# Kernel tuning notes

Hardware: AMD Instinct MI355X
Metric: run time of the kernel (lower is better)

## Reference

```python
import jax, jax.numpy as jnp
import numpy as np

EPS = 1e-06

def setup_inputs() -> dict:
    key = jax.random.key(0)
    k1, k2, k3, k4 = jax.random.split(key, 4)
    B, N, H, W = 8, 8, 512, 512
    pd_rgbo = jax.random.normal(k1, (B, 4, H, W), dtype=jnp.float32)
    gt_rgbo = jax.random.normal(k2, (B, 4, H, W), dtype=jnp.float32)
    pd_mask = jax.random.randint(k3, (B, N, H, W), 0, 2, dtype=jnp.int32)
    gt_mask = jax.random.randint(k4, (B, N, H, W), 0, 2, dtype=jnp.int32)
    return {"pd_rgbo": pd_rgbo, "gt_rgbo": gt_rgbo, "pd_mask": pd_mask, "gt_mask": gt_mask}

def reference(pd_rgbo, gt_rgbo, pd_mask, gt_mask):
    # masks -> bool, derived mask combinations
    pm = pd_mask.astype(bool)            # [B,N,H,W]
    gm = gt_mask.astype(bool)
    dt = pd_rgbo.dtype
    pmf = pm.astype(dt)
    and_f = (pm & gm).astype(dt)         # logical_and
    xor_f = (pm & ~gm).astype(dt)        # xor(or, gt) == pd & ~gt
    gmf = gm.astype(dt)

    pd_rgb = pd_rgbo[:, :3]              # [B,3,H,W]
    gt_rgb = gt_rgbo[:, :3]
    pd_o = jnp.round(pd_rgbo[:, 3])      # [B,H,W]
    gt_o = jnp.round(gt_rgbo[:, 3])

    # per-pixel L2 color distance over channels: [B,H,W]
    diff_norm = jnp.linalg.norm(pd_rgb - gt_rgb, ord=2, axis=1)

    # punish: mean color distance over predicted-mask pixels (per b,n)
    sim_sum = jnp.einsum('bhw,bnhw->bn', diff_norm, pmf)
    count = jnp.sum(pmf, axis=(2, 3))
    punish = sim_sum / (count + EPS)

    # IoU from rounded opacities masked by logical masks
    inter = jnp.einsum('bhw,bnhw->bn', pd_o, and_f)
    gt_sum = jnp.einsum('bhw,bnhw->bn', gt_o, gmf)
    pd_xor_sum = jnp.einsum('bhw,bnhw->bn', pd_o, xor_f)
    iou = inter / (gt_sum + pd_xor_sum + EPS)

    # weights default to ones -> plain mean over all (b, n) pairs
    loss = jnp.mean(1.0 - iou + punish)
    return loss
```

## Files before the change

### kernel.cpp

```cpp
#include <hip/hip_runtime.h>


constexpr int Bc  = 8;
constexpr int Nc  = 8;
constexpr int HWc = 512 * 512;
constexpr int BPI = 512;
constexpr float EPSc = 1e-6f;

__device__ __forceinline__ float2 gload_f2(const float* a) {
    float2 r;
    asm volatile("global_load_dwordx2 %0, %1, off" : "=v"(r) : "v"(a) : "memory");
    return r;
}
__device__ __forceinline__ int4 gload_i4(const int* a) {
    int4 r;
    asm volatile("global_load_dwordx4 %0, %1, off" : "=v"(r) : "v"(a) : "memory");
    return r;
}
#define WAITV(n_) do {                                                   \
        asm volatile("s_waitcnt vmcnt(" #n_ ")" ::: "memory");           \
        __builtin_amdgcn_sched_barrier(0);                               \
    } while (0)

__device__ __forceinline__ float wave_reduce(float v) {
#pragma unroll
    for (int off = 32; off; off >>= 1) v += __shfl_xor(v, off, 64);
    return v;
}

template<bool USE_PART>
__global__ __launch_bounds__(256, 4) void niou_partial(
    const float* __restrict__ pd, const float* __restrict__ gt,
    const int* __restrict__ pmask, const int* __restrict__ gmask,
    float* __restrict__ outp )
{
    __shared__ float dnL[512], poL[512], goL[512];

    const int tid  = threadIdx.x;
    const int b    = blockIdx.x >> 9;
    const int blk  = blockIdx.x & 511;
    const int base = blk * 512;

    const float* pdB = pd + (size_t)b * 4 * HWc + base + 2 * tid;
    const float* gtB = gt + (size_t)b * 4 * HWc + base + 2 * tid;
    float2 pr[4], gr[4];
#pragma unroll
    for (int c = 0; c < 4; ++c) pr[c] = gload_f2(pdB + (size_t)c * HWc);
#pragma unroll
    for (int c = 0; c < 4; ++c) gr[c] = gload_f2(gtB + (size_t)c * HWc);

    const int g = tid >> 6, q = tid & 63;
    int4 pmv[2][2], gmv[2][2];
#pragma unroll
    for (int pp = 0; pp < 2; ++pp) {
        const size_t pl = (size_t)(b * Nc + 2 * g + pp) * HWc + base + 4 * q;
#pragma unroll
        for (int qq = 0; qq < 2; ++qq) {
            pmv[pp][qq] = gload_i4(pmask + pl + 256 * qq);
            gmv[pp][qq] = gload_i4(gmask + pl + 256 * qq);
        }
    }

    WAITV(8);
    {
        const float dx0 = pr[0].x - gr[0].x, dy0 = pr[1].x - gr[1].x, dz0 = pr[2].x - gr[2].x;
        const float dx1 = pr[0].y - gr[0].y, dy1 = pr[1].y - gr[1].y, dz1 = pr[2].y - gr[2].y;
        float2 d2, p2, g2;
        d2.x = sqrtf(dx0*dx0 + dy0*dy0 + dz0*dz0);
        d2.y = sqrtf(dx1*dx1 + dy1*dy1 + dz1*dz1);
        p2.x = rintf(pr[3].x); p2.y = rintf(pr[3].y);
        g2.x = rintf(gr[3].x); g2.y = rintf(gr[3].y);
        *reinterpret_cast<float2*>(&dnL[2 * tid]) = d2;
        *reinterpret_cast<float2*>(&poL[2 * tid]) = p2;
        *reinterpret_cast<float2*>(&goL[2 * tid]) = g2;
    }
    __syncthreads();

    WAITV(0);
    float4 dnq[2], poq[2], goq[2];
#pragma unroll
    for (int qq = 0; qq < 2; ++qq) {
        const int li = 256 * qq + 4 * q;
        dnq[qq] = *reinterpret_cast<const float4*>(&dnL[li]);
        poq[qq] = *reinterpret_cast<const float4*>(&poL[li]);
        goq[qq] = *reinterpret_cast<const float4*>(&goL[li]);
    }

    float acc[2][4];
    int   wcnt[2];
#pragma unroll
    for (int pp = 0; pp < 2; ++pp) {
        wcnt[pp] = 0;
#pragma unroll
        for (int k = 0; k < 4; ++k) acc[pp][k] = 0.f;
    }

#pragma unroll
    for (int pp = 0; pp < 2; ++pp)
#pragma unroll
        for (int qq = 0; qq < 2; ++qq) {
            const int pmx[4] = {pmv[pp][qq].x, pmv[pp][qq].y, pmv[pp][qq].z, pmv[pp][qq].w};
            const int gmx[4] = {gmv[pp][qq].x, gmv[pp][qq].y, gmv[pp][qq].z, gmv[pp][qq].w};
            const float dnj[4] = {dnq[qq].x, dnq[qq].y, dnq[qq].z, dnq[qq].w};
            const float poj[4] = {poq[qq].x, poq[qq].y, poq[qq].z, poq[qq].w};
            const float goj[4] = {goq[qq].x, goq[qq].y, goq[qq].z, goq[qq].w};
#pragma unroll
            for (int j = 0; j < 4; ++j) {
                const bool P = pmx[j] != 0;
                const bool G = gmx[j] != 0;
                wcnt[pp] += __popcll(__ballot(P));
                const float s = P ? poj[j] : 0.f;
                acc[pp][0] += P ? dnj[j] : 0.f;
                acc[pp][1] += G ? s      : 0.f;
                acc[pp][2] += G ? goj[j] : 0.f;
                acc[pp][3] += s;
            }
        }

    const int lane = tid & 63;
#pragma unroll
    for (int pp = 0; pp < 2; ++pp) {
        const float s0 = wave_reduce(acc[pp][0]);
        const float s1 = wave_reduce(acc[pp][1]);
        const float s2 = wave_reduce(acc[pp][2]);
        const float s3 = wave_reduce(acc[pp][3]);
        if (lane == 0) {
            const int n = 2 * g + pp;
            if (USE_PART) {
                float* dst = outp + (size_t)(b * 40 + n * 5) * BPI + blk;
                dst[0 * BPI] = s0;
                dst[1 * BPI] = (float)wcnt[pp];
                dst[2 * BPI] = s1;
                dst[3 * BPI] = s2;
                dst[4 * BPI] = s3;
            } else {
                float* wsn = outp + (size_t)(b * 40 + n * 5) * 16;
                atomicAdd(&wsn[0 * 16], s0);
                atomicAdd(&wsn[1 * 16], (float)wcnt[pp]);
                atomicAdd(&wsn[2 * 16], s1);
                atomicAdd(&wsn[3 * 16], s2);
                atomicAdd(&wsn[4 * 16], s3);
            }
        }
    }
}

__global__ __launch_bounds__(256) void niou_reduce(
    const float* __restrict__ part, float* __restrict__ sums)
{
    const int slot = blockIdx.x;
    const int tid  = threadIdx.x;
    float s = 0.f;
#pragma unroll
    for (int i = 0; i < BPI; i += 256) s += part[(size_t)slot * BPI + i + tid];
    s = wave_reduce(s);
    __shared__ float w4[4];
    if ((tid & 63) == 0) w4[tid >> 6] = s;
    __syncthreads();
    if (tid == 0) sums[slot] = w4[0] + w4[1] + w4[2] + w4[3];
}

__global__ __launch_bounds__(64) void niou_final(
    const float* __restrict__ w0, float* __restrict__ out, int pad)
{
    const int t = threadIdx.x;
    const float* w = w0 + (size_t)t * 5 * pad;
    const float sim   = w[0 * pad];
    const float cnt   = w[1 * pad];
    const float inter = w[2 * pad];
    const float gts   = w[3 * pad];
    const float ssum  = w[4 * pad];
    const float xo    = ssum - inter;
    const float punish = sim / (cnt + EPSc);
    const float iou    = inter / (gts + xo + EPSc);
    float term = 1.0f - iou + punish;
#pragma unroll
    for (int off = 32; off; off >>= 1) term += __shfl_xor(term, off, 64);
    if (t == 0) out[0] = term * (1.0f / 64.0f);
}

extern "C" void kernel_launch(void* const* d_in, const int* in_sizes, int n_in,
                              void* d_out, int out_size, void* d_ws, size_t ws_size,
                              hipStream_t stream) {
    const float* pd_rgbo = (const float*)d_in[0];
    const float* gt_rgbo = (const float*)d_in[1];
    const int*   pd_mask = (const int*)d_in[2];
    const int*   gt_mask = (const int*)d_in[3];
    float* out = (float*)d_out;
    float* ws  = (float*)d_ws;

    const size_t need = ((size_t)320 * BPI + 320) * sizeof(float);
    if (ws_size >= need) {
        float* part = ws;
        float* sums = ws + (size_t)320 * BPI;
        niou_partial<true><<<Bc * BPI, 256, 0, stream>>>(pd_rgbo, gt_rgbo,
                                                         pd_mask, gt_mask, part);
        niou_reduce<<<320, 256, 0, stream>>>(part, sums);
        niou_final<<<1, 64, 0, stream>>>(sums, out, 1);
    } else {
        hipMemsetAsync(ws, 0, 320 * 16 * sizeof(float), stream);
        niou_partial<false><<<Bc * BPI, 256, 0, stream>>>(pd_rgbo, gt_rgbo,
                                                          pd_mask, gt_mask, ws);
        niou_final<<<1, 64, 0, stream>>>(ws, out, 16);
    }
}
```

Baseline: 38.61 us.

## Replace partial-sum buffer and reduce kernel with atomics; split mask wait

Drops the two-pass reduction (per-block partial writes plus a separate reduce kernel) and always accumulates per-(b,n) sums with float atomics into a zeroed, padded workspace, preceded by a memset. This removes one kernel launch and the partial-buffer traffic, at the cost of contention from 512 blocks atomically adding to each of 320 slots. It also splits the final vmcnt wait so the first mask plane pair is processed while the second is still in flight. Float atomics make the summation order nondeterministic.

Result: slower. 59.00 us (+52.8%).

```diff
diff --git a/kernel.cpp b/kernel.cpp
--- a/kernel.cpp
+++ b/kernel.cpp
@@ -5,6 +5,7 @@
 constexpr int Nc  = 8;
 constexpr int HWc = 512 * 512;
 constexpr int BPI = 512;
+constexpr int PAD = 16;
 constexpr float EPSc = 1e-6f;
 
 __device__ __forceinline__ float2 gload_f2(const float* a) {
@@ -28,11 +29,10 @@
     return v;
 }
 
-template<bool USE_PART>
 __global__ __launch_bounds__(256, 4) void niou_partial(
     const float* __restrict__ pd, const float* __restrict__ gt,
     const int* __restrict__ pmask, const int* __restrict__ gmask,
-    float* __restrict__ outp )
+    float* __restrict__ ws )
 {
     __shared__ float dnL[512], poL[512], goL[512];
 
@@ -76,7 +76,6 @@
     }
     __syncthreads();
 
-    WAITV(0);
     float4 dnq[2], poq[2], goq[2];
 #pragma unroll
     for (int qq = 0; qq < 2; ++qq) {
@@ -96,7 +95,8 @@
     }
 
 #pragma unroll
-    for (int pp = 0; pp < 2; ++pp)
+    for (int pp = 0; pp < 2; ++pp) {
+        if (pp == 0) WAITV(4); else WAITV(0);
 #pragma unroll
         for (int qq = 0; qq < 2; ++qq) {
             const int pmx[4] = {pmv[pp][qq].x, pmv[pp][qq].y, pmv[pp][qq].z, pmv[pp][qq].w};
@@ -116,6 +116,7 @@
                 acc[pp][3] += s;
             }
         }
+    }
 
     const int lane = tid & 63;
 #pragma unroll
@@ -126,50 +127,26 @@
         const float s3 = wave_reduce(acc[pp][3]);
         if (lane == 0) {
             const int n = 2 * g + pp;
-            if (USE_PART) {
-                float* dst = outp + (size_t)(b * 40 + n * 5) * BPI + blk;
-                dst[0 * BPI] = s0;
-                dst[1 * BPI] = (float)wcnt[pp];
-                dst[2 * BPI] = s1;
-                dst[3 * BPI] = s2;
-                dst[4 * BPI] = s3;
-            } else {
-                float* wsn = outp + (size_t)(b * 40 + n * 5) * 16;
-                atomicAdd(&wsn[0 * 16], s0);
-                atomicAdd(&wsn[1 * 16], (float)wcnt[pp]);
-                atomicAdd(&wsn[2 * 16], s1);
-                atomicAdd(&wsn[3 * 16], s2);
-                atomicAdd(&wsn[4 * 16], s3);
-            }
+            float* wsn = ws + (size_t)(b * 40 + n * 5) * PAD;
+            atomicAdd(&wsn[0 * PAD], s0);
+            atomicAdd(&wsn[1 * PAD], (float)wcnt[pp]);
+            atomicAdd(&wsn[2 * PAD], s1);
+            atomicAdd(&wsn[3 * PAD], s2);
+            atomicAdd(&wsn[4 * PAD], s3);
         }
     }
 }
 
-__global__ __launch_bounds__(256) void niou_reduce(
-    const float* __restrict__ part, float* __restrict__ sums)
-{
-    const int slot = blockIdx.x;
-    const int tid  = threadIdx.x;
-    float s = 0.f;
-#pragma unroll
-    for (int i = 0; i < BPI; i += 256) s += part[(size_t)slot * BPI + i + tid];
-    s = wave_reduce(s);
-    __shared__ float w4[4];
-    if ((tid & 63) == 0) w4[tid >> 6] = s;
-    __syncthreads();
-    if (tid == 0) sums[slot] = w4[0] + w4[1] + w4[2] + w4[3];
-}
-
 __global__ __launch_bounds__(64) void niou_final(
-    const float* __restrict__ w0, float* __restrict__ out, int pad)
+    const float* __restrict__ w0, float* __restrict__ out)
 {
     const int t = threadIdx.x;
-    const float* w = w0 + (size_t)t * 5 * pad;
-    const float sim   = w[0 * pad];
-    const float cnt   = w[1 * pad];
-    const float inter = w[2 * pad];
-    const float gts   = w[3 * pad];
-    const float ssum  = w[4 * pad];
+    const float* w = w0 + (size_t)t * 5 * PAD;
+    const float sim   = w[0 * PAD];
+    const float cnt   = w[1 * PAD];
+    const float inter = w[2 * PAD];
+    const float gts   = w[3 * PAD];
+    const float ssum  = w[4 * PAD];
     const float xo    = ssum - inter;
     const float punish = sim / (cnt + EPSc);
     const float iou    = inter / (gts + xo + EPSc);
@@ -189,18 +166,7 @@
     float* out = (float*)d_out;
     float* ws  = (float*)d_ws;
 
-    const size_t need = ((size_t)320 * BPI + 320) * sizeof(float);
-    if (ws_size >= need) {
-        float* part = ws;
-        float* sums = ws + (size_t)320 * BPI;
-        niou_partial<true><<<Bc * BPI, 256, 0, stream>>>(pd_rgbo, gt_rgbo,
-                                                         pd_mask, gt_mask, part);
-        niou_reduce<<<320, 256, 0, stream>>>(part, sums);
-        niou_final<<<1, 64, 0, stream>>>(sums, out, 1);
-    } else {
-        hipMemsetAsync(ws, 0, 320 * 16 * sizeof(float), stream);
-        niou_partial<false><<<Bc * BPI, 256, 0, stream>>>(pd_rgbo, gt_rgbo,
-                                                          pd_mask, gt_mask, ws);
-        niou_final<<<1, 64, 0, stream>>>(ws, out, 16);
-    }
+    hipMemsetAsync(ws, 0, Bc * 40 * PAD * sizeof(float), stream);
+    niou_partial<<<Bc * BPI, 256, 0, stream>>>(pd_rgbo, gt_rgbo, pd_mask, gt_mask, ws);
+    niou_final<<<1, 64, 0, stream>>>(ws, out);
 }
```

## Process two pixel chunks per block with second-chunk loads overlapping first compute

Applied to the files above, without the earlier changes.

Each block now covers 1024 pixels in two 512-pixel chunks, so the grid is half as large. The second chunk's colour and mask loads are issued before the first chunk is processed, and double-buffered shared arrays with staged vmcnt waits let them overlap. The aim is more memory parallelism per wave and less per-block setup and tail overhead in a bandwidth-bound kernel. The cost is more live registers, a second barrier per block, and fewer blocks to spread across the GPU.

New measurement: 40.40 us. +4.6%, slower.

```diff
diff --git a/kernel.cpp b/kernel.cpp
--- a/kernel.cpp
+++ b/kernel.cpp
@@ -4,7 +4,7 @@
 constexpr int Bc  = 8;
 constexpr int Nc  = 8;
 constexpr int HWc = 512 * 512;
-constexpr int BPI = 512;
+constexpr int BPI = 256;
 constexpr float EPSc = 1e-6f;
 
 __device__ __forceinline__ float2 gload_f2(const float* a) {
@@ -34,57 +34,61 @@
     const int* __restrict__ pmask, const int* __restrict__ gmask,
     float* __restrict__ outp )
 {
-    __shared__ float dnL[512], poL[512], goL[512];
+    __shared__ float dnL[2][512], poL[2][512], goL[2][512];
 
     const int tid  = threadIdx.x;
-    const int b    = blockIdx.x >> 9;
-    const int blk  = blockIdx.x & 511;
-    const int base = blk * 512;
-
-    const float* pdB = pd + (size_t)b * 4 * HWc + base + 2 * tid;
-    const float* gtB = gt + (size_t)b * 4 * HWc + base + 2 * tid;
-    float2 pr[4], gr[4];
-#pragma unroll
-    for (int c = 0; c < 4; ++c) pr[c] = gload_f2(pdB + (size_t)c * HWc);
-#pragma unroll
-    for (int c = 0; c < 4; ++c) gr[c] = gload_f2(gtB + (size_t)c * HWc);
-
-    const int g = tid >> 6, q = tid & 63;
-    int4 pmv[2][2], gmv[2][2];
-#pragma unroll
-    for (int pp = 0; pp < 2; ++pp) {
-        const size_t pl = (size_t)(b * Nc + 2 * g + pp) * HWc + base + 4 * q;
-#pragma unroll
-        for (int qq = 0; qq < 2; ++qq) {
-            pmv[pp][qq] = gload_i4(pmask + pl + 256 * qq);
-            gmv[pp][qq] = gload_i4(gmask + pl + 256 * qq);
-        }
+    const int b    = blockIdx.x >> 8;
+    const int blk  = blockIdx.x & 255;
+    const int base = blk * 1024;
+    const int g    = tid >> 6, q = tid & 63;
+
+    const float* pdI = pd + (size_t)b * 4 * HWc + base;
+    const float* gtI = gt + (size_t)b * 4 * HWc + base;
+    const size_t mpl0 = (size_t)(b * Nc + 2 * g    ) * HWc + base + 4 * q;
+    const size_t mpl1 = (size_t)(b * Nc + 2 * g + 1) * HWc + base + 4 * q;
+
+    float2 pr0[4], gr0[4];
+#pragma unroll
+    for (int c = 0; c < 4; ++c) pr0[c] = gload_f2(pdI + (size_t)c * HWc + 2 * tid);
+#pragma unroll
+    for (int c = 0; c < 4; ++c) gr0[c] = gload_f2(gtI + (size_t)c * HWc + 2 * tid);
+    int4 pmv0[2][2], gmv0[2][2];
+#pragma unroll
+    for (int qq = 0; qq < 2; ++qq) {
+        pmv0[0][qq] = gload_i4(pmask + mpl0 + 256 * qq);
+        gmv0[0][qq] = gload_i4(gmask + mpl0 + 256 * qq);
+        pmv0[1][qq] = gload_i4(pmask + mpl1 + 256 * qq);
+        gmv0[1][qq] = gload_i4(gmask + mpl1 + 256 * qq);
     }
 
     WAITV(8);
     {
-        const float dx0 = pr[0].x - gr[0].x, dy0 = pr[1].x - gr[1].x, dz0 = pr[2].x - gr[2].x;
-        const float dx1 = pr[0].y - gr[0].y, dy1 = pr[1].y - gr[1].y, dz1 = pr[2].y - gr[2].y;
+        const float dx0 = pr0[0].x - gr0[0].x, dy0 = pr0[1].x - gr0[1].x, dz0 = pr0[2].x - gr0[2].x;
+        const float dx1 = pr0[0].y - gr0[0].y, dy1 = pr0[1].y - gr0[1].y, dz1 = pr0[2].y - gr0[2].y;
         float2 d2, p2, g2;
         d2.x = sqrtf(dx0*dx0 + dy0*dy0 + dz0*dz0);
         d2.y = sqrtf(dx1*dx1 + dy1*dy1 + dz1*dz1);
-        p2.x = rintf(pr[3].x); p2.y = rintf(pr[3].y);
-        g2.x = rintf(gr[3].x); g2.y = rintf(gr[3].y);
-        *reinterpret_cast<float2*>(&dnL[2 * tid]) = d2;
-        *reinterpret_cast<float2*>(&poL[2 * tid]) = p2;
-        *reinterpret_cast<float2*>(&goL[2 * tid]) = g2;
+        p2.x = rintf(pr0[3].x); p2.y = rintf(pr0[3].y);
+        g2.x = rintf(gr0[3].x); g2.y = rintf(gr0[3].y);
+        *reinterpret_cast<float2*>(&dnL[0][2 * tid]) = d2;
+        *reinterpret_cast<float2*>(&poL[0][2 * tid]) = p2;
+        *reinterpret_cast<float2*>(&goL[0][2 * tid]) = g2;
+    }
+
+    float2 pr1[4], gr1[4];
+#pragma unroll
+    for (int c = 0; c < 4; ++c) pr1[c] = gload_f2(pdI + (size_t)c * HWc + 512 + 2 * tid);
+#pragma unroll
+    for (int c = 0; c < 4; ++c) gr1[c] = gload_f2(gtI + (size_t)c * HWc + 512 + 2 * tid);
+    int4 pmv1[2][2], gmv1[2][2];
+#pragma unroll
+    for (int qq = 0; qq < 2; ++qq) {
+        pmv1[0][qq] = gload_i4(pmask + mpl0 + 512 + 256 * qq);
+        gmv1[0][qq] = gload_i4(gmask + mpl0 + 512 + 256 * qq);
+        pmv1[1][qq] = gload_i4(pmask + mpl1 + 512 + 256 * qq);
+        gmv1[1][qq] = gload_i4(gmask + mpl1 + 512 + 256 * qq);
     }
     __syncthreads();
-
-    WAITV(0);
-    float4 dnq[2], poq[2], goq[2];
-#pragma unroll
-    for (int qq = 0; qq < 2; ++qq) {
-        const int li = 256 * qq + 4 * q;
-        dnq[qq] = *reinterpret_cast<const float4*>(&dnL[li]);
-        poq[qq] = *reinterpret_cast<const float4*>(&poL[li]);
-        goq[qq] = *reinterpret_cast<const float4*>(&goL[li]);
-    }
 
     float acc[2][4];
     int   wcnt[2];
@@ -95,27 +99,56 @@
         for (int k = 0; k < 4; ++k) acc[pp][k] = 0.f;
     }
 
-#pragma unroll
-    for (int pp = 0; pp < 2; ++pp)
-#pragma unroll
-        for (int qq = 0; qq < 2; ++qq) {
-            const int pmx[4] = {pmv[pp][qq].x, pmv[pp][qq].y, pmv[pp][qq].z, pmv[pp][qq].w};
-            const int gmx[4] = {gmv[pp][qq].x, gmv[pp][qq].y, gmv[pp][qq].z, gmv[pp][qq].w};
-            const float dnj[4] = {dnq[qq].x, dnq[qq].y, dnq[qq].z, dnq[qq].w};
-            const float poj[4] = {poq[qq].x, poq[qq].y, poq[qq].z, poq[qq].w};
-            const float goj[4] = {goq[qq].x, goq[qq].y, goq[qq].z, goq[qq].w};
-#pragma unroll
-            for (int j = 0; j < 4; ++j) {
-                const bool P = pmx[j] != 0;
-                const bool G = gmx[j] != 0;
-                wcnt[pp] += __popcll(__ballot(P));
-                const float s = P ? poj[j] : 0.f;
-                acc[pp][0] += P ? dnj[j] : 0.f;
-                acc[pp][1] += G ? s      : 0.f;
-                acc[pp][2] += G ? goj[j] : 0.f;
-                acc[pp][3] += s;
-            }
+#define PROCESS(pmv_, gmv_, it_)                                              \
+    _Pragma("unroll")                                                         \
+    for (int pp = 0; pp < 2; ++pp)                                            \
+        _Pragma("unroll")                                                     \
+        for (int qq = 0; qq < 2; ++qq) {                                      \
+            const int li = 256 * qq + 4 * q;                                  \
+            const float4 dnq = *reinterpret_cast<const float4*>(&dnL[it_][li]);\
+            const float4 poq = *reinterpret_cast<const float4*>(&poL[it_][li]);\
+            const float4 goq = *reinterpret_cast<const float4*>(&goL[it_][li]);\
+            const int pmx[4] = {pmv_[pp][qq].x, pmv_[pp][qq].y,               \
+                                pmv_[pp][qq].z, pmv_[pp][qq].w};              \
+            const int gmx[4] = {gmv_[pp][qq].x, gmv_[pp][qq].y,               \
+                                gmv_[pp][qq].z, gmv_[pp][qq].w};              \
+            const float dnj[4] = {dnq.x, dnq.y, dnq.z, dnq.w};                \
+            const float poj[4] = {poq.x, poq.y, poq.z, poq.w};                \
+            const float goj[4] = {goq.x, goq.y, goq.z, goq.w};                \
+            _Pragma("unroll")                                                 \
+            for (int j = 0; j < 4; ++j) {                                     \
+                const bool P = pmx[j] != 0;                                   \
+                const bool G = gmx[j] != 0;                                   \
+                wcnt[pp] += __popcll(__ballot(P));                            \
+                const float s = P ? poj[j] : 0.f;                             \
+                acc[pp][0] += P ? dnj[j] : 0.f;                               \
+                acc[pp][1] += G ? s      : 0.f;                               \
+                acc[pp][2] += G ? goj[j] : 0.f;                               \
+                acc[pp][3] += s;                                              \
+            }                                                                 \
         }
+
+    WAITV(16);
+    PROCESS(pmv0, gmv0, 0)
+
+    WAITV(8);
+    {
+        const float dx0 = pr1[0].x - gr1[0].x, dy0 = pr1[1].x - gr1[1].x, dz0 = pr1[2].x - gr1[2].x;
+        const float dx1 = pr1[0].y - gr1[0].y, dy1 = pr1[1].y - gr1[1].y, dz1 = pr1[2].y - gr1[2].y;
+        float2 d2, p2, g2;
+        d2.x = sqrtf(dx0*dx0 + dy0*dy0 + dz0*dz0);
+        d2.y = sqrtf(dx1*dx1 + dy1*dy1 + dz1*dz1);
+        p2.x = rintf(pr1[3].x); p2.y = rintf(pr1[3].y);
+        g2.x = rintf(gr1[3].x); g2.y = rintf(gr1[3].y);
+        *reinterpret_cast<float2*>(&dnL[1][2 * tid]) = d2;
+        *reinterpret_cast<float2*>(&poL[1][2 * tid]) = p2;
+        *reinterpret_cast<float2*>(&goL[1][2 * tid]) = g2;
+    }
+    __syncthreads();
+
+    WAITV(0);
+    PROCESS(pmv1, gmv1, 1)
+#undef PROCESS
 
     const int lane = tid & 63;
 #pragma unroll
@@ -152,7 +185,8 @@
     const int tid  = threadIdx.x;
     float s = 0.f;
 #pragma unroll
-    for (int i = 0; i < BPI; i += 256) s += part[(size_t)slot * BPI + i + tid];
+    for (int i = 0; i < BPI; i += 256)
+        if (i + tid < BPI) s += part[(size_t)slot * BPI + i + tid];
     s = wave_reduce(s);
     __shared__ float w4[4];
     if ((tid & 63) == 0) w4[tid >> 6] = s;
```

## Merge reduce and final kernels via last-block ticket; split mask waitcnt

Applied to the files above, without the earlier changes.

Replaces the separate per-slot reduce kernel and single-block final kernel with one tail kernel. Each of its 64 blocks reduces the five partial rows for one (b,n) pair and computes that pair's loss term, and the last block to finish (found through an atomic ticket) averages the terms. This removes one kernel launch but adds a memset for the ticket. The partial kernel also waits only on the first half of the mask loads before processing them, so compute on the first mask pair can overlap the remaining loads.

Measured after the change: 45.18 us. 1.17x slower.

```diff
diff --git a/kernel.cpp b/kernel.cpp
--- a/kernel.cpp
+++ b/kernel.cpp
@@ -76,7 +76,6 @@
     }
     __syncthreads();
 
-    WAITV(0);
     float4 dnq[2], poq[2], goq[2];
 #pragma unroll
     for (int qq = 0; qq < 2; ++qq) {
@@ -96,7 +95,8 @@
     }
 
 #pragma unroll
-    for (int pp = 0; pp < 2; ++pp)
+    for (int pp = 0; pp < 2; ++pp) {
+        if (pp == 0) WAITV(4); else WAITV(0);
 #pragma unroll
         for (int qq = 0; qq < 2; ++qq) {
             const int pmx[4] = {pmv[pp][qq].x, pmv[pp][qq].y, pmv[pp][qq].z, pmv[pp][qq].w};
@@ -116,6 +116,7 @@
                 acc[pp][3] += s;
             }
         }
+    }
 
     const int lane = tid & 63;
 #pragma unroll
@@ -145,31 +146,62 @@
     }
 }
 
-__global__ __launch_bounds__(256) void niou_reduce(
-    const float* __restrict__ part, float* __restrict__ sums)
+__global__ __launch_bounds__(256) void niou_tail(
+    const float* __restrict__ part, float* __restrict__ sums,
+    unsigned int* __restrict__ ticket, float* __restrict__ out)
 {
-    const int slot = blockIdx.x;
-    const int tid  = threadIdx.x;
-    float s = 0.f;
-#pragma unroll
-    for (int i = 0; i < BPI; i += 256) s += part[(size_t)slot * BPI + i + tid];
-    s = wave_reduce(s);
-    __shared__ float w4[4];
-    if ((tid & 63) == 0) w4[tid >> 6] = s;
+    const int bn  = blockIdx.x;
+    const int tid = threadIdx.x;
+
+    float loc[5];
+#pragma unroll
+    for (int s = 0; s < 5; ++s) {
+        const float* row = part + ((size_t)bn * 5 + s) * BPI;
+        loc[s] = row[tid] + row[tid + 256];
+        loc[s] = wave_reduce(loc[s]);
+    }
+
+    __shared__ float red[4][5];
+    __shared__ bool  last;
+    if ((tid & 63) == 0) {
+#pragma unroll
+        for (int s = 0; s < 5; ++s) red[tid >> 6][s] = loc[s];
+    }
     __syncthreads();
-    if (tid == 0) sums[slot] = w4[0] + w4[1] + w4[2] + w4[3];
-}
-
-__global__ __launch_bounds__(64) void niou_final(
-    const float* __restrict__ w0, float* __restrict__ out, int pad)
+
+    if (tid == 0) {
+        const float sim   = red[0][0] + red[1][0] + red[2][0] + red[3][0];
+        const float cnt   = red[0][1] + red[1][1] + red[2][1] + red[3][1];
+        const float inter = red[0][2] + red[1][2] + red[2][2] + red[3][2];
+        const float gts   = red[0][3] + red[1][3] + red[2][3] + red[3][3];
+        const float ssum  = red[0][4] + red[1][4] + red[2][4] + red[3][4];
+        const float xo    = ssum - inter;
+        const float punish = sim / (cnt + EPSc);
+        const float iou    = inter / (gts + xo + EPSc);
+        sums[bn] = 1.0f - iou + punish;
+        __threadfence();
+        last = (atomicAdd(ticket, 1u) == 63u);
+    }
+    __syncthreads();
+
+    if (last && tid < 64) {
+        float term = __hip_atomic_load(&sums[tid], __ATOMIC_RELAXED,
+                                       __HIP_MEMORY_SCOPE_AGENT);
+        term = wave_reduce(term);
+        if (tid == 0) out[0] = term * (1.0f / 64.0f);
+    }
+}
+
+__global__ __launch_bounds__(64) void niou_final_fb(
+    const float* __restrict__ w0, float* __restrict__ out)
 {
     const int t = threadIdx.x;
-    const float* w = w0 + (size_t)t * 5 * pad;
-    const float sim   = w[0 * pad];
-    const float cnt   = w[1 * pad];
-    const float inter = w[2 * pad];
-    const float gts   = w[3 * pad];
-    const float ssum  = w[4 * pad];
+    const float* w = w0 + (size_t)t * 5 * 16;
+    const float sim   = w[0 * 16];
+    const float cnt   = w[1 * 16];
+    const float inter = w[2 * 16];
+    const float gts   = w[3 * 16];
+    const float ssum  = w[4 * 16];
     const float xo    = ssum - inter;
     const float punish = sim / (cnt + EPSc);
     const float iou    = inter / (gts + xo + EPSc);
@@ -189,18 +221,20 @@
     float* out = (float*)d_out;
     float* ws  = (float*)d_ws;
 
-    const size_t need = ((size_t)320 * BPI + 320) * sizeof(float);
+    const size_t partN = (size_t)320 * BPI;
+    const size_t need  = (partN + 64 + 1) * sizeof(float);
     if (ws_size >= need) {
         float* part = ws;
-        float* sums = ws + (size_t)320 * BPI;
+        float* sums = ws + partN;
+        unsigned int* ticket = (unsigned int*)(ws + partN + 64);
+        hipMemsetAsync(ticket, 0, sizeof(unsigned int), stream);
         niou_partial<true><<<Bc * BPI, 256, 0, stream>>>(pd_rgbo, gt_rgbo,
                                                          pd_mask, gt_mask, part);
-        niou_reduce<<<320, 256, 0, stream>>>(part, sums);
-        niou_final<<<1, 64, 0, stream>>>(sums, out, 1);
+        niou_tail<<<64, 256, 0, stream>>>(part, sums, ticket, out);
     } else {
         hipMemsetAsync(ws, 0, 320 * 16 * sizeof(float), stream);
         niou_partial<false><<<Bc * BPI, 256, 0, stream>>>(pd_rgbo, gt_rgbo,
                                                           pd_mask, gt_mask, ws);
-        niou_final<<<1, 64, 0, stream>>>(ws, out, 16);
-    }
-}
+        niou_final_fb<<<1, 64, 0, stream>>>(ws, out);
+    }
+}
```
